# Performance work log

Hardware: AMD Instinct MI355X
Metric: run time of the kernel (lower is better)

Reference implementation:

```python
import jax, jax.numpy as jnp
import numpy as np

MARGIN = 0.3  # init kwarg, mode='norm'


def _pairwise_dist(X):
    # squared euclidean distances, then safe sqrt (matches euc_dist(X.t()).sqrt())
    sq = jnp.sum(X * X, axis=1)                      # [n]
    d2 = sq[:, None] + sq[None, :] - 2.0 * (X @ X.T)  # [n, n]
    d2 = jnp.maximum(d2, 0.0)
    # safe sqrt: avoid inf derivative at 0 (diagonal); forward value identical
    return jnp.where(d2 > 0.0, jnp.sqrt(jnp.where(d2 > 0.0, d2, 1.0)), 0.0)


def setup_inputs() -> dict:
    key = jax.random.key(0)
    kx, ky = jax.random.split(key)
    X = jax.random.normal(kx, (4096, 2048), dtype=jnp.float32)
    Y = jax.random.randint(ky, (4096,), 0, 128, dtype=jnp.int64)
    return {"X": X, "Y": Y}


def reference(X, Y):
    dist = _pairwise_dist(X)                         # [n, n]
    mask = Y[:, None] == Y[None, :]                  # same-identity mask [n, n]
    inf = jnp.array(jnp.inf, dtype=dist.dtype)
    # hardest positive per anchor: max over same-label entries
    dist_ap = jnp.max(jnp.where(mask, dist, -inf), axis=1)  # [n]
    # hardest negative per anchor: min over different-label entries
    dist_an = jnp.min(jnp.where(mask, inf, dist), axis=1)   # [n]
    # mode == 'norm': mean hinge
    return jnp.mean(jnp.maximum(dist_ap - dist_an + MARGIN, 0.0))
```

## Files before the change

kernel.cpp:

```cpp
#include <hip/hip_runtime.h>
#include <hip/hip_bf16.h>
#include <hip/hip_fp8.h>

typedef __attribute__((ext_vector_type(4))) int i32x4;
typedef __attribute__((ext_vector_type(8))) int i32x8;
typedef __attribute__((ext_vector_type(16))) float f32x16;

#define MARGIN 0.3f
#define BIGF 3.0e38f

__device__ __forceinline__ f32x16 mx_mfma(i32x8 a, i32x8 b, f32x16 c) {
    return __builtin_amdgcn_mfma_scale_f32_32x32x64_f8f6f4(
        a, b, c, 0 , 0 ,
        0, 127 , 0, 127 );
}

__device__ __forceinline__ i32x8 ld32(const unsigned char* p) {
    i32x4 lo = *(const i32x4*)p;
    i32x4 hi = *(const i32x4*)(p + 16);
    return __builtin_shufflevector(lo, hi, 0, 1, 2, 3, 4, 5, 6, 7);
}

__global__ __launch_bounds__(256) void convert_norm_kernel(
    const float* __restrict__ X, unsigned char* __restrict__ Xf,
    float* __restrict__ nrm, unsigned* __restrict__ ap,
    unsigned* __restrict__ an, unsigned* __restrict__ cnt, int K) {
    const int wave = threadIdx.x >> 6, lane = threadIdx.x & 63;
    const int row = blockIdx.x * 4 + wave;
    const float* xr = X + (size_t)row * K;
    const size_t pbase = ((size_t)(row >> 5)) << 16;
    const int rsub = row & 31;
    float s = 0.0f;
    for (int c = lane * 8; c < K; c += 64 * 8) {
        float4 v0 = *(const float4*)(xr + c);
        float4 v1 = *(const float4*)(xr + c + 4);
        float f[8] = {v0.x, v0.y, v0.z, v0.w, v1.x, v1.y, v1.z, v1.w};
        union { unsigned char b[8]; uint2 u; } p;
#pragma unroll
        for (int i = 0; i < 8; i++) {
            __hip_fp8_e4m3 q(f[i]);
            p.b[i] = q.__x;
            float d = (float)q;
            s += d * d;
        }
        const int lslot = rsub + (((c >> 5) & 1) << 5);
        unsigned char* dst = Xf + pbase + ((size_t)(c >> 6) << 11)
                             + (lslot << 5) + (c & 31);
        *(uint2*)dst = p.u;
    }
    for (int off = 32; off > 0; off >>= 1) s += __shfl_xor(s, off, 64);
    if (lane == 0) {
        nrm[row] = s;
        ap[row] = 0u;
        an[row] = 0x7F800000u;
        if (row == 0) *cnt = 0u;
    }
}

__global__ __launch_bounds__(256, 2) void gemm_reduce_kernel(
    const unsigned char* __restrict__ Xf, const float* __restrict__ nrm,
    const int* __restrict__ Y, unsigned* __restrict__ ap,
    unsigned* __restrict__ an, unsigned* __restrict__ cnt,
    float* __restrict__ out, int N, int K) {
    __shared__ int sYr[256], sYc[128];
    __shared__ float sNr[256], sNc[128];
    __shared__ float lsum[4];
    __shared__ unsigned s_done;

    const int tid = threadIdx.x;
    const int wave = tid >> 6;
    const int lane = tid & 63;
    const int m = lane & 31;
    const int h = lane >> 5;

    const int rowBase = (blockIdx.x >> 5) << 8;
    const int colBase = (blockIdx.x & 31) << 7;

    if (tid < 256) {
        sYr[tid] = Y[rowBase + tid];
        sNr[tid] = nrm[rowBase + tid];
    }
    if (tid < 128) {
        sYc[tid] = Y[colBase + tid];
        sNc[tid] = nrm[colBase + tid];
    }

    f32x16 acc[2][4];
#pragma unroll
    for (int si = 0; si < 2; si++)
#pragma unroll
        for (int sj = 0; sj < 4; sj++)
#pragma unroll
            for (int rr = 0; rr < 16; rr++) acc[si][sj][rr] = 0.0f;

    const unsigned char* pa[2];
    const unsigned char* pb[4];
#pragma unroll
    for (int si = 0; si < 2; si++)
        pa[si] = Xf + (((size_t)(rowBase >> 5) + wave * 2 + si) << 16) + lane * 32;
#pragma unroll
    for (int sj = 0; sj < 4; sj++)
        pb[sj] = Xf + (((size_t)(colBase >> 5) + sj) << 16) + lane * 32;

    i32x8 A0[2], B0[4], A1[2], B1[4];

#define LD(Ab, Bb, t)                                                   \
    do {                                                                \
        const size_t _o = (size_t)(t) << 11;                            \
        _Pragma("unroll") for (int _i = 0; _i < 2; _i++)                \
            Ab[_i] = ld32(pa[_i] + _o);                                 \
        _Pragma("unroll") for (int _j = 0; _j < 4; _j++)                \
            Bb[_j] = ld32(pb[_j] + _o);                                 \
    } while (0)

#define MM(Ab, Bb)                                                      \
    do {                                                                \
        _Pragma("unroll") for (int _i = 0; _i < 2; _i++)                \
            _Pragma("unroll") for (int _j = 0; _j < 4; _j++)            \
                acc[_i][_j] = mx_mfma(Ab[_i], Bb[_j], acc[_i][_j]);     \
    } while (0)

    const int nt = K >> 6;
    LD(A0, B0, 0);
    int t = 0;
    for (; t + 2 < nt; t += 2) {
        LD(A1, B1, t + 1);
        MM(A0, B0);
        LD(A0, B0, t + 2);
        MM(A1, B1);
    }
    LD(A1, B1, t + 1);
    MM(A0, B0);
    MM(A1, B1);

#undef LD
#undef MM

    __syncthreads();

#pragma unroll
    for (int si = 0; si < 2; si++)
#pragma unroll
        for (int reg = 0; reg < 16; reg++) {
            const int row64 = si * 32 + (reg & 3) + 8 * (reg >> 2) + 4 * h;
            const int rIdx = wave * 64 + row64;
            const int yr = sYr[rIdx];
            const float nr = sNr[rIdx];
            float dp = -1.0f, dn = BIGF;
#pragma unroll
            for (int sj = 0; sj < 4; sj++) {
                const int cIdx = sj * 32 + m;
                float d2 = nr + sNc[cIdx] - 2.0f * acc[si][sj][reg];
                float d = sqrtf(fmaxf(d2, 0.0f));
                bool same = (yr == sYc[cIdx]);
                dp = fmaxf(dp, same ? d : -1.0f);
                dn = fminf(dn, same ? BIGF : d);
            }
            for (int off = 1; off < 32; off <<= 1) {
                dp = fmaxf(dp, __shfl_xor(dp, off, 64));
                dn = fminf(dn, __shfl_xor(dn, off, 64));
            }
            if (m == 0) {
                atomicMax(&ap[rowBase + rIdx], __float_as_uint(fmaxf(dp, 0.0f)));
                atomicMin(&an[rowBase + rIdx], __float_as_uint(dn));
            }
        }

    __syncthreads();
    if (tid == 0) {
        __threadfence();
        s_done = atomicAdd(cnt, 1u);
    }
    __syncthreads();
    if (s_done == gridDim.x - 1) {
        __threadfence();
        float s = 0.0f;
        for (int i = tid; i < N; i += 256) {
            unsigned ua = __hip_atomic_load(&ap[i], __ATOMIC_RELAXED,
                                            __HIP_MEMORY_SCOPE_AGENT);
            unsigned ub = __hip_atomic_load(&an[i], __ATOMIC_RELAXED,
                                            __HIP_MEMORY_SCOPE_AGENT);
            s += fmaxf(__uint_as_float(ua) - __uint_as_float(ub) + MARGIN, 0.0f);
        }
        for (int off = 32; off > 0; off >>= 1) s += __shfl_xor(s, off, 64);
        if (lane == 0) lsum[wave] = s;
        __syncthreads();
        if (tid == 0)
            out[0] = (lsum[0] + lsum[1] + lsum[2] + lsum[3]) / (float)N;
    }
}

extern "C" void kernel_launch(void* const* d_in, const int* in_sizes, int n_in,
                              void* d_out, int out_size, void* d_ws, size_t ws_size,
                              hipStream_t stream) {
    const float* X = (const float*)d_in[0];
    const int* Y = (const int*)d_in[1];
    float* out = (float*)d_out;
    const int N = in_sizes[1];
    const int K = in_sizes[0] / N;

    char* ws = (char*)d_ws;
    unsigned char* Xf = (unsigned char*)ws;
    float* nrm = (float*)(ws + (size_t)N * K);
    unsigned* ap = (unsigned*)((char*)nrm + (size_t)N * 4);
    unsigned* an = (unsigned*)((char*)ap + (size_t)N * 4);
    unsigned* cnt = (unsigned*)((char*)an + (size_t)N * 4);

    convert_norm_kernel<<<N / 4, 256, 0, stream>>>(X, Xf, nrm, ap, an, cnt, K);
    const int NBr = N / 256, NBc = N / 128;
    gemm_reduce_kernel<<<NBr * NBc, 256, 0, stream>>>(Xf, nrm, Y, ap, an, cnt,
                                                      out, N, K);
}
```

Measured before the change: 128.6 us.

## Exploit distance-matrix symmetry by computing only upper-triangular 64x64 tiles

The fused GEMM-reduce now launches one single-wave block per upper-triangular 64x64 tile of the pairwise distance matrix instead of covering the full square. Each tile folds its results into the row hardest positive/negative and also, via column-wise reductions, into the column entries. This roughly halves the FP8 MFMA work and operand traffic. In exchange it adds more atomics per tile, drops the LDS staging of labels and norms in favour of direct global reads, uses smaller per-wave tiles with less reuse, and maps block index to tile with a serial search.

```diff
diff --git a/kernel.cpp b/kernel.cpp
--- a/kernel.cpp
+++ b/kernel.cpp
@@ -57,66 +57,56 @@
     }
 }
 
-__global__ __launch_bounds__(256, 2) void gemm_reduce_kernel(
+__global__ __launch_bounds__(64, 4) void gemm_reduce_kernel(
     const unsigned char* __restrict__ Xf, const float* __restrict__ nrm,
     const int* __restrict__ Y, unsigned* __restrict__ ap,
     unsigned* __restrict__ an, unsigned* __restrict__ cnt,
     float* __restrict__ out, int N, int K) {
-    __shared__ int sYr[256], sYc[128];
-    __shared__ float sNr[256], sNc[128];
-    __shared__ float lsum[4];
     __shared__ unsigned s_done;
 
-    const int tid = threadIdx.x;
-    const int wave = tid >> 6;
-    const int lane = tid & 63;
+    const int lane = threadIdx.x;
     const int m = lane & 31;
     const int h = lane >> 5;
 
-    const int rowBase = (blockIdx.x >> 5) << 8;
-    const int colBase = (blockIdx.x & 31) << 7;
-
-    if (tid < 256) {
-        sYr[tid] = Y[rowBase + tid];
-        sNr[tid] = nrm[rowBase + tid];
-    }
-    if (tid < 128) {
-        sYc[tid] = Y[colBase + tid];
-        sNc[tid] = nrm[colBase + tid];
-    }
-
-    f32x16 acc[2][4];
+    const int NB2 = N >> 6;
+    int bi = blockIdx.x, ti = 0;
+    while (bi >= NB2 - ti) { bi -= NB2 - ti; ti++; }
+    const int tj = ti + bi;
+    const int rowBase = ti << 6;
+    const int colBase = tj << 6;
+
+    f32x16 acc[2][2];
 #pragma unroll
     for (int si = 0; si < 2; si++)
 #pragma unroll
-        for (int sj = 0; sj < 4; sj++)
+        for (int sj = 0; sj < 2; sj++)
 #pragma unroll
             for (int rr = 0; rr < 16; rr++) acc[si][sj][rr] = 0.0f;
 
     const unsigned char* pa[2];
-    const unsigned char* pb[4];
+    const unsigned char* pb[2];
 #pragma unroll
     for (int si = 0; si < 2; si++)
-        pa[si] = Xf + (((size_t)(rowBase >> 5) + wave * 2 + si) << 16) + lane * 32;
-#pragma unroll
-    for (int sj = 0; sj < 4; sj++)
-        pb[sj] = Xf + (((size_t)(colBase >> 5) + sj) << 16) + lane * 32;
-
-    i32x8 A0[2], B0[4], A1[2], B1[4];
+        pa[si] = Xf + (((size_t)(ti * 2 + si)) << 16) + lane * 32;
+#pragma unroll
+    for (int sj = 0; sj < 2; sj++)
+        pb[sj] = Xf + (((size_t)(tj * 2 + sj)) << 16) + lane * 32;
+
+    i32x8 A0[2], B0[2], A1[2], B1[2];
 
 #define LD(Ab, Bb, t)                                                   \
     do {                                                                \
         const size_t _o = (size_t)(t) << 11;                            \
         _Pragma("unroll") for (int _i = 0; _i < 2; _i++)                \
             Ab[_i] = ld32(pa[_i] + _o);                                 \
-        _Pragma("unroll") for (int _j = 0; _j < 4; _j++)                \
+        _Pragma("unroll") for (int _j = 0; _j < 2; _j++)                \
             Bb[_j] = ld32(pb[_j] + _o);                                 \
     } while (0)
 
 #define MM(Ab, Bb)                                                      \
     do {                                                                \
         _Pragma("unroll") for (int _i = 0; _i < 2; _i++)                \
-            _Pragma("unroll") for (int _j = 0; _j < 4; _j++)            \
+            _Pragma("unroll") for (int _j = 0; _j < 2; _j++)            \
                 acc[_i][_j] = mx_mfma(Ab[_i], Bb[_j], acc[_i][_j]);     \
     } while (0)
 
@@ -136,38 +126,61 @@
 #undef LD
 #undef MM
 
-    __syncthreads();
-
+    const int gc0 = colBase + m, gc1 = colBase + 32 + m;
+    const int yc0 = Y[gc0], yc1 = Y[gc1];
+    const float nc0 = nrm[gc0], nc1 = nrm[gc1];
+
+    float cdp0 = -1.0f, cdp1 = -1.0f;
+    float cdn0 = BIGF, cdn1 = BIGF;
 #pragma unroll
     for (int si = 0; si < 2; si++)
 #pragma unroll
         for (int reg = 0; reg < 16; reg++) {
             const int row64 = si * 32 + (reg & 3) + 8 * (reg >> 2) + 4 * h;
-            const int rIdx = wave * 64 + row64;
-            const int yr = sYr[rIdx];
-            const float nr = sNr[rIdx];
-            float dp = -1.0f, dn = BIGF;
-#pragma unroll
-            for (int sj = 0; sj < 4; sj++) {
-                const int cIdx = sj * 32 + m;
-                float d2 = nr + sNc[cIdx] - 2.0f * acc[si][sj][reg];
+            const int gr = rowBase + row64;
+            const int yr = Y[gr];
+            const float nr = nrm[gr];
+            float dp, dn;
+            {
+                float d2 = nr + nc0 - 2.0f * acc[si][0][reg];
                 float d = sqrtf(fmaxf(d2, 0.0f));
-                bool same = (yr == sYc[cIdx]);
-                dp = fmaxf(dp, same ? d : -1.0f);
-                dn = fminf(dn, same ? BIGF : d);
+                bool same = (yr == yc0);
+                float vp = same ? d : -1.0f;
+                float vn = same ? BIGF : d;
+                dp = vp; dn = vn;
+                cdp0 = fmaxf(cdp0, vp); cdn0 = fminf(cdn0, vn);
+            }
+            {
+                float d2 = nr + nc1 - 2.0f * acc[si][1][reg];
+                float d = sqrtf(fmaxf(d2, 0.0f));
+                bool same = (yr == yc1);
+                float vp = same ? d : -1.0f;
+                float vn = same ? BIGF : d;
+                dp = fmaxf(dp, vp); dn = fminf(dn, vn);
+                cdp1 = fmaxf(cdp1, vp); cdn1 = fminf(cdn1, vn);
             }
             for (int off = 1; off < 32; off <<= 1) {
                 dp = fmaxf(dp, __shfl_xor(dp, off, 64));
                 dn = fminf(dn, __shfl_xor(dn, off, 64));
             }
             if (m == 0) {
-                atomicMax(&ap[rowBase + rIdx], __float_as_uint(fmaxf(dp, 0.0f)));
-                atomicMin(&an[rowBase + rIdx], __float_as_uint(dn));
+                atomicMax(&ap[gr], __float_as_uint(fmaxf(dp, 0.0f)));
+                atomicMin(&an[gr], __float_as_uint(dn));
             }
         }
+    cdp0 = fmaxf(cdp0, __shfl_xor(cdp0, 32, 64));
+    cdn0 = fminf(cdn0, __shfl_xor(cdn0, 32, 64));
+    cdp1 = fmaxf(cdp1, __shfl_xor(cdp1, 32, 64));
+    cdn1 = fminf(cdn1, __shfl_xor(cdn1, 32, 64));
+    if (h == 0) {
+        atomicMax(&ap[gc0], __float_as_uint(fmaxf(cdp0, 0.0f)));
+        atomicMin(&an[gc0], __float_as_uint(cdn0));
+        atomicMax(&ap[gc1], __float_as_uint(fmaxf(cdp1, 0.0f)));
+        atomicMin(&an[gc1], __float_as_uint(cdn1));
+    }
 
     __syncthreads();
-    if (tid == 0) {
+    if (lane == 0) {
         __threadfence();
         s_done = atomicAdd(cnt, 1u);
     }
@@ -175,7 +188,7 @@
     if (s_done == gridDim.x - 1) {
         __threadfence();
         float s = 0.0f;
-        for (int i = tid; i < N; i += 256) {
+        for (int i = lane; i < N; i += 64) {
             unsigned ua = __hip_atomic_load(&ap[i], __ATOMIC_RELAXED,
                                             __HIP_MEMORY_SCOPE_AGENT);
             unsigned ub = __hip_atomic_load(&an[i], __ATOMIC_RELAXED,
@@ -183,10 +196,7 @@
             s += fmaxf(__uint_as_float(ua) - __uint_as_float(ub) + MARGIN, 0.0f);
         }
         for (int off = 32; off > 0; off >>= 1) s += __shfl_xor(s, off, 64);
-        if (lane == 0) lsum[wave] = s;
-        __syncthreads();
-        if (tid == 0)
-            out[0] = (lsum[0] + lsum[1] + lsum[2] + lsum[3]) / (float)N;
+        if (lane == 0) out[0] = s / (float)N;
     }
 }
 
@@ -207,7 +217,8 @@
     unsigned* cnt = (unsigned*)((char*)an + (size_t)N * 4);
 
     convert_norm_kernel<<<N / 4, 256, 0, stream>>>(X, Xf, nrm, ap, an, cnt, K);
-    const int NBr = N / 256, NBc = N / 128;
-    gemm_reduce_kernel<<<NBr * NBc, 256, 0, stream>>>(Xf, nrm, Y, ap, an, cnt,
-                                                      out, N, K);
-}
+    const int NB2 = N / 64;
+    const int ntri = NB2 * (NB2 + 1) / 2;
+    gemm_reduce_kernel<<<ntri, 64, 0, stream>>>(Xf, nrm, Y, ap, an, cnt,
+                                                out, N, K);
+}
```

Result: slower. 189.6 us (+47.4%).
